# Optimization experiments

Hardware: AMD Instinct MI355X
Metric: run time of the kernel (lower is better)

Reference implementation:

```python
import jax, jax.numpy as jnp
import numpy as np

IMAGE_MAX_DIM = 1024.0
POOL_H, POOL_W = 7, 7
LEVEL_THRESH = 48.0


def crop_and_resize(image, boxes, box_idx, crop_h, crop_w):
    """Faithful jax port of tf.image.crop_and_resize (bilinear, extrapolation 0).
    image: [B,H,W,C]; boxes: [N,4] normalized (y1,x1,y2,x2); box_idx: [N] int32.
    Returns [N,crop_h,crop_w,C].
    """
    B, H, W, C = image.shape
    y1, x1, y2, x2 = boxes[:, 0], boxes[:, 1], boxes[:, 2], boxes[:, 3]
    ry = jnp.arange(crop_h, dtype=boxes.dtype) / (crop_h - 1)  # [ph]
    rx = jnp.arange(crop_w, dtype=boxes.dtype) / (crop_w - 1)  # [pw]
    # TF: in_y = y1*(H-1) + i*(y2-y1)*(H-1)/(ph-1)
    ys = (y1[:, None] + ry[None, :] * (y2 - y1)[:, None]) * (H - 1)  # [N,ph]
    xs = (x1[:, None] + rx[None, :] * (x2 - x1)[:, None]) * (W - 1)  # [N,pw]
    y0f = jnp.floor(ys)
    x0f = jnp.floor(xs)
    wy = ys - y0f  # [N,ph]
    wx = xs - x0f  # [N,pw]
    y0 = jnp.clip(y0f, 0, H - 1).astype(jnp.int32)
    yp = jnp.clip(y0f + 1, 0, H - 1).astype(jnp.int32)
    x0 = jnp.clip(x0f, 0, W - 1).astype(jnp.int32)
    xp = jnp.clip(x0f + 1, 0, W - 1).astype(jnp.int32)
    b = box_idx[:, None, None]  # [N,1,1]

    def gather(yy, xx):
        # [N,ph,pw,C] corner gather
        return image[b, yy[:, :, None], xx[:, None, :]]

    wxe = wx[:, None, :, None]  # [N,1,pw,1]
    top = gather(y0, x0) * (1.0 - wxe) + gather(y0, xp) * wxe
    bot = gather(yp, x0) * (1.0 - wxe) + gather(yp, xp) * wxe
    wye = wy[:, :, None, None]  # [N,ph,1,1]
    out = top * (1.0 - wye) + bot * wye
    # extrapolation_value = 0 outside the image
    valid = ((ys >= 0) & (ys <= H - 1))[:, :, None] & ((xs >= 0) & (xs <= W - 1))[:, None, :]
    return jnp.where(valid[..., None], out, jnp.zeros((), dtype=out.dtype))


def setup_inputs() -> dict:
    key = jax.random.key(0)
    k0, k1, k2, k3 = jax.random.split(key, 4)
    B, R, C = 2, 512, 256
    feat0 = jax.random.normal(k0, (B, 256, 256, C), dtype=jnp.float32)
    feat1 = jax.random.normal(k1, (B, 128, 128, C), dtype=jnp.float32)
    # boxes in pixel coords within a 1024x1024 image; sizes 8..128 so both
    # levels (threshold 48 px) are exercised
    tl = jax.random.uniform(k2, (B, R, 2), minval=0.0, maxval=896.0)
    hw = jax.random.uniform(k3, (B, R, 2), minval=8.0, maxval=128.0)
    rois = jnp.concatenate([tl, tl + hw, jnp.zeros((B, R, 1))], axis=-1).astype(jnp.float32)
    return {"feat0": feat0, "feat1": feat1, "rois": rois}


def reference(feat0, feat1, rois):
    B, R = rois.shape[:2]
    C = feat0.shape[-1]
    boxes = rois[..., :4].reshape(B * R, 4)  # pixel coords (y1,x1,y2,x2)
    h = boxes[:, 2] - boxes[:, 0]
    w = boxes[:, 3] - boxes[:, 1]
    # level 1 iff h>48 or w>48 (the scatter_nd of ones), else level 0
    level = (h > LEVEL_THRESH) | (w > LEVEL_THRESH)  # [B*R] bool
    nboxes = jax.lax.stop_gradient(boxes / IMAGE_MAX_DIM)
    box_idx = jnp.repeat(jnp.arange(B, dtype=jnp.int32), R)
    c0 = crop_and_resize(feat0, nboxes, box_idx, POOL_H, POOL_W)
    c1 = crop_and_resize(feat1, nboxes, box_idx, POOL_H, POOL_W)
    # per-box level select replaces the gather/concat/sort/gather reorder chain
    # (which merely restores original (batch, roi) order)
    pooled = jnp.where(level[:, None, None, None], c1, c0)
    return pooled.reshape(B, R, POOL_H, POOL_W, C)
```

## Files before the change

### kernel.cpp

```cpp
#include <hip/hip_runtime.h>


#define POOL 7
#define NCH 256

typedef float v4f __attribute__((ext_vector_type(4)));

__global__ __launch_bounds__(256) void roialign_kernel(
    const float* __restrict__ feat0,
    const float* __restrict__ feat1,
    const float* __restrict__ rois,
    float* __restrict__ out,
    int NB, int R)
{
    int n = blockIdx.x;
    if (n >= NB) return;
    int lane = threadIdx.x & 63;
    int wave = threadIdx.x >> 6;

    const float* roi = rois + (size_t)n * 5;
    float y1 = roi[0], x1 = roi[1], y2 = roi[2], x2 = roi[3];

    bool lvl = (y2 - y1 > 48.0f) || (x2 - x1 > 48.0f);
    const float* feat = lvl ? feat1 : feat0;
    int H = lvl ? 128 : 256;
    int W = H;
    int b = n / R;

    const float inv_img = 1.0f / 1024.0f;
    float y1n = y1 * inv_img, y2n = y2 * inv_img;
    float x1n = x1 * inv_img, x2n = x2 * inv_img;
    float Hm1 = (float)(H - 1), Wm1 = (float)(W - 1);
    float dy = y2n - y1n, dx = x2n - x1n;

    size_t plane = (size_t)b * H * W;
    int coff = lane * 4;
    float* outbase = out + (size_t)n * 49 * NCH + coff;

    for (int p = wave; p < 49; p += 4) {
        int i = p / POOL;
        int j = p - i * POOL;

        float ys = (y1n + ((float)i / 6.0f) * dy) * Hm1;
        float xs = (x1n + ((float)j / 6.0f) * dx) * Wm1;

        float y0f = floorf(ys), x0f = floorf(xs);
        float wy = ys - y0f;
        float wx = xs - x0f;

        int y0 = (int)fminf(fmaxf(y0f,        0.0f), Hm1);
        int yp = (int)fminf(fmaxf(y0f + 1.0f, 0.0f), Hm1);
        int x0 = (int)fminf(fmaxf(x0f,        0.0f), Wm1);
        int xp = (int)fminf(fmaxf(x0f + 1.0f, 0.0f), Wm1);

        bool valid = (ys >= 0.0f) && (ys <= Hm1) && (xs >= 0.0f) && (xs <= Wm1);

        size_t r0 = (plane + (size_t)y0 * W) * NCH;
        size_t r1 = (plane + (size_t)yp * W) * NCH;

        v4f v00 = *(const v4f*)(feat + r0 + (size_t)x0 * NCH + coff);
        v4f v01 = *(const v4f*)(feat + r0 + (size_t)xp * NCH + coff);
        v4f v10 = *(const v4f*)(feat + r1 + (size_t)x0 * NCH + coff);
        v4f v11 = *(const v4f*)(feat + r1 + (size_t)xp * NCH + coff);

        float wx1 = 1.0f - wx, wy1 = 1.0f - wy;
        v4f top = v00 * wx1 + v01 * wx;
        v4f bot = v10 * wx1 + v11 * wx;
        v4f o   = top * wy1 + bot * wy;
        if (!valid) o = (v4f)0.0f;

        *(v4f*)(outbase + (size_t)p * NCH) = o;
    }
}

extern "C" void kernel_launch(void* const* d_in, const int* in_sizes, int n_in,
                              void* d_out, int out_size, void* d_ws, size_t ws_size,
                              hipStream_t stream) {
    const float* feat0 = (const float*)d_in[0];
    const float* feat1 = (const float*)d_in[1];
    const float* rois  = (const float*)d_in[2];
    float* out = (float*)d_out;

    int B  = in_sizes[0] / (256 * 256 * 256);
    int NB = in_sizes[2] / 5;
    int R  = NB / B;

    roialign_kernel<<<NB, 256, 0, stream>>>(feat0, feat1, rois, out, NB, R);
}
```

Baseline: 214.5 us.

## Remap work so each wave handles two bins with all eight loads issued together

Each wave now processes two pooled bins of one ROI, giving 25 waves per ROI in a flat grid, instead of one block of four waves looping over 49 bins. All eight corner loads are issued before any arithmetic, so more memory requests are in flight per wave. The grid grows to many more waves, which raises the number of loads outstanding at once. In exchange, the ROI setup and level selection are repeated in every wave, and the last wave of each ROI handles only one bin, leaving it half idle.

Measured after the change: 208.9 us. -2.6%, faster.

```diff
diff --git a/kernel.cpp b/kernel.cpp
--- a/kernel.cpp
+++ b/kernel.cpp
@@ -13,10 +13,15 @@
     float* __restrict__ out,
     int NB, int R)
 {
-    int n = blockIdx.x;
+    int t = blockIdx.x * blockDim.x + threadIdx.x;
+    int lane = t & 63;
+    int wid  = t >> 6;
+    int n    = wid / 25;
     if (n >= NB) return;
-    int lane = threadIdx.x & 63;
-    int wave = threadIdx.x >> 6;
+    int q    = wid - n * 25;
+    int p0   = q * 2;
+    bool has2 = (q < 24);
+    int p1   = has2 ? p0 + 1 : p0;
 
     const float* roi = rois + (size_t)n * 5;
     float y1 = roi[0], x1 = roi[1], y2 = roi[2], x2 = roi[3];
@@ -37,39 +42,56 @@
     int coff = lane * 4;
     float* outbase = out + (size_t)n * 49 * NCH + coff;
 
-    for (int p = wave; p < 49; p += 4) {
-        int i = p / POOL;
-        int j = p - i * POOL;
+    int i0 = p0 / POOL, j0 = p0 - i0 * POOL;
+    float ys0 = (y1n + ((float)i0 / 6.0f) * dy) * Hm1;
+    float xs0 = (x1n + ((float)j0 / 6.0f) * dx) * Wm1;
+    float y0f0 = floorf(ys0), x0f0 = floorf(xs0);
+    float wy0 = ys0 - y0f0, wx0 = xs0 - x0f0;
+    int ya0 = (int)fminf(fmaxf(y0f0,        0.0f), Hm1);
+    int yb0 = (int)fminf(fmaxf(y0f0 + 1.0f, 0.0f), Hm1);
+    int xa0 = (int)fminf(fmaxf(x0f0,        0.0f), Wm1);
+    int xb0 = (int)fminf(fmaxf(x0f0 + 1.0f, 0.0f), Wm1);
+    bool valid0 = (ys0 >= 0.0f) && (ys0 <= Hm1) && (xs0 >= 0.0f) && (xs0 <= Wm1);
+    size_t r00 = (plane + (size_t)ya0 * W) * NCH;
+    size_t r10 = (plane + (size_t)yb0 * W) * NCH;
 
-        float ys = (y1n + ((float)i / 6.0f) * dy) * Hm1;
-        float xs = (x1n + ((float)j / 6.0f) * dx) * Wm1;
+    int i1 = p1 / POOL, j1 = p1 - i1 * POOL;
+    float ys1 = (y1n + ((float)i1 / 6.0f) * dy) * Hm1;
+    float xs1 = (x1n + ((float)j1 / 6.0f) * dx) * Wm1;
+    float y0f1 = floorf(ys1), x0f1 = floorf(xs1);
+    float wy1w = ys1 - y0f1, wx1w = xs1 - x0f1;
+    int ya1 = (int)fminf(fmaxf(y0f1,        0.0f), Hm1);
+    int yb1 = (int)fminf(fmaxf(y0f1 + 1.0f, 0.0f), Hm1);
+    int xa1 = (int)fminf(fmaxf(x0f1,        0.0f), Wm1);
+    int xb1 = (int)fminf(fmaxf(x0f1 + 1.0f, 0.0f), Wm1);
+    bool valid1 = (ys1 >= 0.0f) && (ys1 <= Hm1) && (xs1 >= 0.0f) && (xs1 <= Wm1);
+    size_t r01 = (plane + (size_t)ya1 * W) * NCH;
+    size_t r11 = (plane + (size_t)yb1 * W) * NCH;
 
-        float y0f = floorf(ys), x0f = floorf(xs);
-        float wy = ys - y0f;
-        float wx = xs - x0f;
+    v4f a00 = *(const v4f*)(feat + r00 + (size_t)xa0 * NCH + coff);
+    v4f a01 = *(const v4f*)(feat + r00 + (size_t)xb0 * NCH + coff);
+    v4f a10 = *(const v4f*)(feat + r10 + (size_t)xa0 * NCH + coff);
+    v4f a11 = *(const v4f*)(feat + r10 + (size_t)xb0 * NCH + coff);
+    v4f b00 = *(const v4f*)(feat + r01 + (size_t)xa1 * NCH + coff);
+    v4f b01 = *(const v4f*)(feat + r01 + (size_t)xb1 * NCH + coff);
+    v4f b10 = *(const v4f*)(feat + r11 + (size_t)xa1 * NCH + coff);
+    v4f b11 = *(const v4f*)(feat + r11 + (size_t)xb1 * NCH + coff);
 
-        int y0 = (int)fminf(fmaxf(y0f,        0.0f), Hm1);
-        int yp = (int)fminf(fmaxf(y0f + 1.0f, 0.0f), Hm1);
-        int x0 = (int)fminf(fmaxf(x0f,        0.0f), Wm1);
-        int xp = (int)fminf(fmaxf(x0f + 1.0f, 0.0f), Wm1);
-
-        bool valid = (ys >= 0.0f) && (ys <= Hm1) && (xs >= 0.0f) && (xs <= Wm1);
-
-        size_t r0 = (plane + (size_t)y0 * W) * NCH;
-        size_t r1 = (plane + (size_t)yp * W) * NCH;
-
-        v4f v00 = *(const v4f*)(feat + r0 + (size_t)x0 * NCH + coff);
-        v4f v01 = *(const v4f*)(feat + r0 + (size_t)xp * NCH + coff);
-        v4f v10 = *(const v4f*)(feat + r1 + (size_t)x0 * NCH + coff);
-        v4f v11 = *(const v4f*)(feat + r1 + (size_t)xp * NCH + coff);
-
-        float wx1 = 1.0f - wx, wy1 = 1.0f - wy;
-        v4f top = v00 * wx1 + v01 * wx;
-        v4f bot = v10 * wx1 + v11 * wx;
-        v4f o   = top * wy1 + bot * wy;
-        if (!valid) o = (v4f)0.0f;
-
-        *(v4f*)(outbase + (size_t)p * NCH) = o;
+    {
+        float wxc = 1.0f - wx0, wyc = 1.0f - wy0;
+        v4f top = a00 * wxc + a01 * wx0;
+        v4f bot = a10 * wxc + a11 * wx0;
+        v4f o   = top * wyc + bot * wy0;
+        if (!valid0) o = (v4f)0.0f;
+        *(v4f*)(outbase + (size_t)p0 * NCH) = o;
+    }
+    if (has2) {
+        float wxc = 1.0f - wx1w, wyc = 1.0f - wy1w;
+        v4f top = b00 * wxc + b01 * wx1w;
+        v4f bot = b10 * wxc + b11 * wx1w;
+        v4f o   = top * wyc + bot * wy1w;
+        if (!valid1) o = (v4f)0.0f;
+        *(v4f*)(outbase + (size_t)p1 * NCH) = o;
     }
 }
 
@@ -85,5 +107,8 @@
     int NB = in_sizes[2] / 5;
     int R  = NB / B;
 
-    roialign_kernel<<<NB, 256, 0, stream>>>(feat0, feat1, rois, out, NB, R);
+    long long threads = (long long)NB * 25 * 64;
+    int block = 256;
+    int grid = (int)((threads + block - 1) / block);
+    roialign_kernel<<<grid, block, 0, stream>>>(feat0, feat1, rois, out, NB, R);
 }
```

## Remap work to 13 waves per ROI with batched 16-load gather

Applied to the files above, without the earlier changes.

Replaces one-block-per-ROI with a flat grid in which each wave handles four consecutive pooled cells of one ROI, giving 13 waves per ROI and packing waves from different ROIs into the same block. All 16 corner loads for a wave's four cells are issued up front, before any interpolation, to raise memory-level parallelism and hide gather latency. The cost is higher register pressure from holding 16 vector loads, plus a small amount of redundant clamped work on the final partial wave.

Measured after the change: 209.0 us. 2.6% less time.

```diff
diff --git a/kernel.cpp b/kernel.cpp
--- a/kernel.cpp
+++ b/kernel.cpp
@@ -3,6 +3,7 @@
 
 #define POOL 7
 #define NCH 256
+#define WPB 13
 
 typedef float v4f __attribute__((ext_vector_type(4)));
 
@@ -13,10 +14,14 @@
     float* __restrict__ out,
     int NB, int R)
 {
-    int n = blockIdx.x;
+    int t = blockIdx.x * blockDim.x + threadIdx.x;
+    int lane = t & 63;
+    int wid  = t >> 6;
+    int n    = wid / WPB;
     if (n >= NB) return;
-    int lane = threadIdx.x & 63;
-    int wave = threadIdx.x >> 6;
+    int q     = wid - n * WPB;
+    int pbase = q * 4;
+    int cnt   = 49 - pbase; if (cnt > 4) cnt = 4;
 
     const float* roi = rois + (size_t)n * 5;
     float y1 = roi[0], x1 = roi[1], y2 = roi[2], x2 = roi[3];
@@ -37,39 +42,51 @@
     int coff = lane * 4;
     float* outbase = out + (size_t)n * 49 * NCH + coff;
 
-    for (int p = wave; p < 49; p += 4) {
-        int i = p / POOL;
-        int j = p - i * POOL;
+    float wyv[4], wxv[4];
+    bool validv[4];
+    const float* addr[4][4];
+
+    #pragma unroll
+    for (int k = 0; k < 4; ++k) {
+        int p = pbase + k; if (p > 48) p = 48;
+        int i = p / POOL, j = p - i * POOL;
 
         float ys = (y1n + ((float)i / 6.0f) * dy) * Hm1;
         float xs = (x1n + ((float)j / 6.0f) * dx) * Wm1;
+        float y0f = floorf(ys), x0f = floorf(xs);
+        wyv[k] = ys - y0f;
+        wxv[k] = xs - x0f;
+        int ya = (int)fminf(fmaxf(y0f,        0.0f), Hm1);
+        int yb = (int)fminf(fmaxf(y0f + 1.0f, 0.0f), Hm1);
+        int xa = (int)fminf(fmaxf(x0f,        0.0f), Wm1);
+        int xb = (int)fminf(fmaxf(x0f + 1.0f, 0.0f), Wm1);
+        validv[k] = (ys >= 0.0f) && (ys <= Hm1) && (xs >= 0.0f) && (xs <= Wm1);
+        size_t r0 = (plane + (size_t)ya * W) * NCH;
+        size_t r1 = (plane + (size_t)yb * W) * NCH;
+        addr[k][0] = feat + r0 + (size_t)xa * NCH + coff;
+        addr[k][1] = feat + r0 + (size_t)xb * NCH + coff;
+        addr[k][2] = feat + r1 + (size_t)xa * NCH + coff;
+        addr[k][3] = feat + r1 + (size_t)xb * NCH + coff;
+    }
 
-        float y0f = floorf(ys), x0f = floorf(xs);
-        float wy = ys - y0f;
-        float wx = xs - x0f;
+    v4f v[4][4];
+    #pragma unroll
+    for (int k = 0; k < 4; ++k)
+        #pragma unroll
+        for (int s = 0; s < 4; ++s)
+            v[k][s] = *(const v4f*)addr[k][s];
 
-        int y0 = (int)fminf(fmaxf(y0f,        0.0f), Hm1);
-        int yp = (int)fminf(fmaxf(y0f + 1.0f, 0.0f), Hm1);
-        int x0 = (int)fminf(fmaxf(x0f,        0.0f), Wm1);
-        int xp = (int)fminf(fmaxf(x0f + 1.0f, 0.0f), Wm1);
-
-        bool valid = (ys >= 0.0f) && (ys <= Hm1) && (xs >= 0.0f) && (xs <= Wm1);
-
-        size_t r0 = (plane + (size_t)y0 * W) * NCH;
-        size_t r1 = (plane + (size_t)yp * W) * NCH;
-
-        v4f v00 = *(const v4f*)(feat + r0 + (size_t)x0 * NCH + coff);
-        v4f v01 = *(const v4f*)(feat + r0 + (size_t)xp * NCH + coff);
-        v4f v10 = *(const v4f*)(feat + r1 + (size_t)x0 * NCH + coff);
-        v4f v11 = *(const v4f*)(feat + r1 + (size_t)xp * NCH + coff);
-
-        float wx1 = 1.0f - wx, wy1 = 1.0f - wy;
-        v4f top = v00 * wx1 + v01 * wx;
-        v4f bot = v10 * wx1 + v11 * wx;
-        v4f o   = top * wy1 + bot * wy;
-        if (!valid) o = (v4f)0.0f;
-
-        *(v4f*)(outbase + (size_t)p * NCH) = o;
+    #pragma unroll
+    for (int k = 0; k < 4; ++k) {
+        if (k < cnt) {
+            float wx = wxv[k], wy = wyv[k];
+            float wxc = 1.0f - wx, wyc = 1.0f - wy;
+            v4f top = v[k][0] * wxc + v[k][1] * wx;
+            v4f bot = v[k][2] * wxc + v[k][3] * wx;
+            v4f o   = top * wyc + bot * wy;
+            if (!validv[k]) o = (v4f)0.0f;
+            *(v4f*)(outbase + (size_t)(pbase + k) * NCH) = o;
+        }
     }
 }
 
@@ -85,5 +102,8 @@
     int NB = in_sizes[2] / 5;
     int R  = NB / B;
 
-    roialign_kernel<<<NB, 256, 0, stream>>>(feat0, feat1, rois, out, NB, R);
+    long long threads = (long long)NB * WPB * 64;
+    int block = 256;
+    int grid = (int)((threads + block - 1) / block);
+    roialign_kernel<<<grid, block, 0, stream>>>(feat0, feat1, rois, out, NB, R);
 }
```
